# Optimization experiments

Measured on AMD Instinct MI355X. Metric: run time of the kernel, lower is better.

Reference implementation:

```python
import jax, jax.numpy as jnp
import numpy as np

# ---- static config ----
G = 4          # num graphs
NG = 512       # nodes per graph
N = G * NG     # total nodes
E = 32768      # num edges
IN_DIM = 128
HID = 32
HEADS = 4
HC = HID * HEADS  # 128
OUT_DIM = 32
N_LAYERS = 2
GRID = 500
Q = 20
NEG_SLOPE = 0.2
QUANTILES = jnp.asarray(np.linspace(0.0, 1.0, Q), jnp.float32)  # [Q]


def setup_inputs() -> dict:
    key = jax.random.key(0)
    ks = jax.random.split(key, 32)
    inp = {}
    inp['x'] = jax.random.normal(ks[0], (N, IN_DIM), jnp.float32)
    inp['edge_index'] = jax.random.randint(ks[1], (2, E), 0, N).astype(jnp.int64)
    inp['batch'] = (jnp.arange(N) // NG).astype(jnp.int64)
    # GATConv params (2 layers, both 128 -> 4 heads x 32, concat)
    for l, (kin,) in enumerate([(IN_DIM,), (HC,)]):
        s = 1.0 / np.sqrt(kin)
        inp[f'W{l}'] = jax.random.normal(ks[2 + 4 * l], (kin, HC), jnp.float32) * s
        inp[f'as{l}'] = jax.random.normal(ks[3 + 4 * l], (HEADS, HID), jnp.float32) * s
        inp[f'ad{l}'] = jax.random.normal(ks[4 + 4 * l], (HEADS, HID), jnp.float32) * s
        inp[f'b{l}'] = jnp.zeros((HC,), jnp.float32)
    for l in range(N_LAYERS + 1):
        inp[f'lpW{l}'] = jax.random.normal(ks[10 + 2 * l], (HC, OUT_DIM), jnp.float32) * (1.0 / np.sqrt(HC))
        inp[f'lpb{l}'] = jnp.zeros((OUT_DIM,), jnp.float32)
    for l in range(N_LAYERS + 1):
        inp[f'kW{l}'] = jax.random.normal(ks[16 + 2 * l], (HC * Q, OUT_DIM), jnp.float32) * (1.0 / np.sqrt(HC * Q))
        inp[f'kb{l}'] = jnp.zeros((OUT_DIM,), jnp.float32)
    inp['pool_w'] = jnp.ones((2,), jnp.float32) / 2.0
    inp['beta'] = jax.random.normal(ks[22], (OUT_DIM,), jnp.float32)
    inp['h0'] = jax.random.normal(ks[23], (1,), jnp.float32)
    return inp


def _gat_layer(x, src, dst, W, a_src, a_dst, bias):
    # PyG GATConv (concat=True, add_self_loops=True, negative_slope=0.2), eval mode
    n = x.shape[0]
    xh = (x @ W).reshape(n, HEADS, HID)              # [N,H,C]
    loop = jnp.arange(n)
    s = jnp.concatenate([src, loop])                 # [E+N]
    d = jnp.concatenate([dst, loop])
    al_s = jnp.einsum('nhc,hc->nh', xh, a_src)       # [N,H]
    al_d = jnp.einsum('nhc,hc->nh', xh, a_dst)
    e = jax.nn.leaky_relu(al_s[s] + al_d[d], NEG_SLOPE)   # [E+N,H]
    e_max = jax.ops.segment_max(e, d, num_segments=n)     # stable softmax per dst
    e = jnp.exp(e - e_max[d])
    denom = jax.ops.segment_sum(e, d, num_segments=n)
    alpha = e / (denom[d] + 1e-16)                   # [E+N,H]
    out = jax.ops.segment_sum(alpha[:, :, None] * xh[s], d, num_segments=n)
    return out.reshape(n, HC) + bias


def _kde_per_graph(xg):
    # xg: [Ng, D] -> [D*Q] soft-quantile features via grid KDE
    n = xg.shape[0]
    mn = xg.min(axis=0) - 1e-6                       # [D]
    mx = xg.max(axis=0) + 1e-6
    grid = jnp.linspace(0.0, 1.0, GRID)[:, None] * (mx - mn) + mn   # [Gp,D]
    std = xg.std(axis=0) + 1e-8 / 3
    h = 1.06 * std * float(n) ** (-0.2)              # [D]
    u = (grid[:, None, :] - xg[None, :, :]) / h      # [Gp,Ng,D]  (dominant tensor)
    kern = jnp.exp(-0.5 * u * u) / (h * np.sqrt(2.0 * np.pi))
    density = kern.mean(axis=1)                      # [Gp,D]
    cdf = jnp.cumsum(density, axis=0)
    cdf = cdf / jnp.clip(cdf[-1:], 1e-8)
    dist = jnp.abs(cdf[:, :, None] - QUANTILES)      # [Gp,D,Q]
    w = jax.nn.sigmoid(-100.0 * dist)
    w = w / (w.sum(axis=0, keepdims=True) + 1e-8)
    qv = (grid[:, :, None] * w).sum(axis=0)          # [D,Q]
    return qv.reshape(-1)


def _readout(cur, lpW, lpb, kW, kb, pool_w):
    xr = cur.reshape(G, NG, -1)
    pooled = jnp.stack([xr.mean(axis=1), xr.max(axis=1)], axis=0)   # [2,G,D]
    wp = (pooled * pool_w[:, None, None]).sum(axis=0)               # [G,D]
    h = wp @ lpW + lpb                                              # [G,out]
    kf = jax.vmap(_kde_per_graph)(xr)                               # [G,D*Q]
    return h, kf @ kW + kb


def reference(x, edge_index, batch, W0, as0, ad0, b0, W1, as1, ad1, b1,
              lpW0, lpb0, lpW1, lpb1, lpW2, lpb2,
              kW0, kb0, kW1, kb1, kW2, kb2, pool_w, beta, h0):
    src, dst = edge_index[0], edge_index[1]
    convs = [(W0, as0, ad0, b0), (W1, as1, ad1, b1)]
    lps = [(lpW0, lpb0), (lpW1, lpb1), (lpW2, lpb2)]
    kps = [(kW0, kb0), (kW1, kb1), (kW2, kb2)]
    cur = x
    h_list, kde_list = [], []
    for i in range(N_LAYERS):
        h, kp = _readout(cur, lps[i][0], lps[i][1], kps[i][0], kps[i][1], pool_w)
        h_list.append(h); kde_list.append(kp)
        cur = _gat_layer(cur, src, dst, *convs[i])
        if i != N_LAYERS - 1:
            cur = jax.nn.relu(cur)
    h, kp = _readout(cur, lps[-1][0], lps[-1][1], kps[-1][0], kps[-1][1], pool_w)
    h_list.append(h); kde_list.append(kp)
    main_out = jnp.stack(h_list).mean(axis=0)        # [G,out]
    kde_out = jnp.stack(kde_list).mean(axis=0)
    risk = (main_out + kde_out) @ beta + h0          # [G]
    return risk
```

## Files before the change

### kernel.cpp

```cpp
#include <hip/hip_runtime.h>
#include <math.h>

#define GNUM 4
#define NG 512
#define NN 2048
#define EE 32768
#define HC 128
#define HEADS 4
#define HID 32
#define GRID_PTS 500
#define QN 20
#define ODIM 32
#define MAXE 160

#define LOG2E 1.44269504088896340736f
#define NEG_HALF_LOG2E -0.72134752044448170368f
#define N_POW_M02 0.2871745887492588f
#define SIG_K 144.269504089f

typedef float v2f __attribute__((ext_vector_type(2)));

__device__ __forceinline__ float fexp2(float x){ return __builtin_amdgcn_exp2f(x); }
__device__ __forceinline__ float frcp(float x){ return __builtin_amdgcn_rcpf(x); }

struct SmemKDE {
  float4 wred4[8];
  float sc[4];
  float wsum[8], woff[9];
  float redw[QN][8], redg[QN][8];
  float qs[QN];
};
struct SmemXW  { float rows[4][HC]; int cnt[4]; };
struct SmemGat {
  int   ssrc[4][MAXE];
  float sexp[4][MAXE][HEADS];
};
union Smem { SmemKDE kde; SmemXW xw; SmemGat gat; };

__device__ void kde_phase(Smem& sm, const float* __restrict__ vpl, const float* __restrict__ spl,
        int b,
        const float* __restrict__ kW, const float* __restrict__ kb, float* __restrict__ kacc,
        const float* __restrict__ lpW, const float* __restrict__ lpb,
        const float* __restrict__ poolw, float* __restrict__ macc){
  int g = b >> 7, d = b & 127;
  int t = threadIdx.x;
  int lane = t & 63, wave = t >> 6;
  size_t base = (size_t)d*NN + g*NG;
  float v  = vpl[base + t];
  float v2 = spl[base + t];
  float mn=v, mx=v, smv=v, sq=v2;
  #pragma unroll
  for (int m=32; m>0; m>>=1){
    mn = fminf(mn, __shfl_xor(mn, m, 64));
    mx = fmaxf(mx, __shfl_xor(mx, m, 64));
    smv += __shfl_xor(smv, m, 64);
    sq += __shfl_xor(sq, m, 64);
  }
  if (lane==0) sm.kde.wred4[wave] = make_float4(mn,mx,smv,sq);
  __syncthreads();
  if (t==0){
    float4 r = sm.kde.wred4[0];
    #pragma unroll
    for (int i=1;i<8;++i){
      float4 bb = sm.kde.wred4[i];
      r.x = fminf(r.x,bb.x); r.y = fmaxf(r.y,bb.y); r.z += bb.z; r.w += bb.w;
    }
    float mean = r.z * (1.f/NG);
    float var  = fmaxf(r.w*(1.f/NG) - mean*mean, 0.f);
    float sd   = sqrtf(var) + (1e-8f/3.f);
    float h    = 1.06f * sd * N_POW_M02;
    float lo = r.x - 1e-6f, hi = r.y + 1e-6f;
    sm.kde.sc[0] = lo;
    sm.kde.sc[1] = (hi-lo)*(1.f/(GRID_PTS-1));
    sm.kde.sc[2] = NEG_HALF_LOG2E/(h*h);
    sm.kde.sc[3] = poolw[0]*mean + poolw[1]*r.y;
  }
  __syncthreads();
  float lo = sm.kde.sc[0], st = sm.kde.sc[1], kk = sm.kde.sc[2];
  float gv = lo + st*(float)t;
  float acc = 0.f;
  {
    float c0 = kk*gv*gv, c1 = -2.f*kk*gv;
    v2f c0v = {c0, c0}, c1v = {c1, c1}, kkv = {kk, kk};
    const float4* pv = (const float4*)(vpl + base);
    const float4* ps = (const float4*)(spl + base);
    #pragma unroll 8
    for (int i=0;i<NG/4;++i){
      float4 a = pv[i];
      float4 bq = ps[i];
      v2f alo = {a.x, a.y}, ahi = {a.z, a.w};
      v2f blo = {bq.x, bq.y}, bhi = {bq.z, bq.w};
      v2f plo = __builtin_elementwise_fma(kkv, blo, __builtin_elementwise_fma(c1v, alo, c0v));
      v2f phi = __builtin_elementwise_fma(kkv, bhi, __builtin_elementwise_fma(c1v, ahi, c0v));
      acc += fexp2(plo.x);
      acc += fexp2(plo.y);
      acc += fexp2(phi.x);
      acc += fexp2(phi.y);
    }
  }
  if (t >= GRID_PTS) acc = 0.f;
  float sv = acc;
  #pragma unroll
  for (int off=1; off<64; off<<=1){
    float n = __shfl_up(sv, off, 64);
    if (lane >= off) sv += n;
  }
  if (lane==63) sm.kde.wsum[wave] = sv;
  __syncthreads();
  if (t==0){
    float r2 = 0.f;
    #pragma unroll
    for (int i=0;i<8;++i){ sm.kde.woff[i]=r2; r2+=sm.kde.wsum[i]; }
    sm.kde.woff[8]=r2;
  }
  if (t < QN*8){ ((float*)sm.kde.redw)[t]=0.f; ((float*)sm.kde.redg)[t]=0.f; }
  __syncthreads();
  float invt = 1.f/fmaxf(sm.kde.woff[8], 1e-8f);
  float c = (sv + sm.kde.woff[wave]) * invt;
  float cw0 = __shfl(c, 0, 64), cw1 = __shfl(c, 63, 64);
  int qlo = max(0, (int)ceilf((cw0 - 0.17f)*(float)(QN-1)));
  int qhi = min(QN-1, (int)floorf((cw1 + 0.17f)*(float)(QN-1)));
  for (int q=qlo; q<=qhi; ++q){
    float w = 0.f;
    if (t < GRID_PTS){
      float dist = fabsf(c - (float)q*(1.f/(QN-1)));
      w = frcp(1.f + fexp2(SIG_K*dist));
    }
    float gw = gv*w;
    #pragma unroll
    for (int m=32;m>0;m>>=1){
      w  += __shfl_xor(w,  m, 64);
      gw += __shfl_xor(gw, m, 64);
    }
    if (lane==0){ sm.kde.redw[q][wave]=w; sm.kde.redg[q][wave]=gw; }
  }
  __syncthreads();
  if (t < QN){
    float sw=0.f, sgw=0.f;
    #pragma unroll
    for (int i=0;i<8;++i){ sw+=sm.kde.redw[t][i]; sgw+=sm.kde.redg[t][i]; }
    sm.kde.qs[t] = sgw / (sw + 1e-8f);
  }
  __syncthreads();
  if (t < ODIM){
    float a = 0.f;
    const float* kwb = kW + (size_t)d*QN*ODIM + t;
    #pragma unroll
    for (int q=0;q<QN;++q) a += sm.kde.qs[q]*kwb[q*ODIM];
    if (d==0) a += kb[t];
    kacc[(size_t)d*128 + g*ODIM + t] = a;
    float bb = sm.kde.sc[3]*lpW[d*ODIM + t];
    if (d==0) bb += lpb[t];
    macc[(size_t)d*128 + g*ODIM + t] = bb;
  }
  __syncthreads();
}

__device__ float gather_core(Smem& sm, int d, int sub, int tl,
        const int* __restrict__ csr, const int* __restrict__ deg,
        const float* __restrict__ als, const float* __restrict__ ald,
        const float* __restrict__ xh, const float* __restrict__ bias){
  int dg = deg[d];
  int E = dg + 1;
  int Ep = (E + 7) & ~7;
  const int* base = csr + d*MAXE;
  float a0 = ald[d*4+0], a1 = ald[d*4+1], a2 = ald[d*4+2], a3 = ald[d*4+3];
  for (int i=tl; i<Ep; i+=128){
    int s = (i < dg) ? base[i] : d;
    sm.gat.ssrc[sub][i] = s;
    if (i < E){
      float e0 = als[s*4+0]+a0, e1 = als[s*4+1]+a1, e2 = als[s*4+2]+a2, e3 = als[s*4+3]+a3;
      e0 = (e0>=0.f)? e0 : 0.2f*e0;
      e1 = (e1>=0.f)? e1 : 0.2f*e1;
      e2 = (e2>=0.f)? e2 : 0.2f*e2;
      e3 = (e3>=0.f)? e3 : 0.2f*e3;
      sm.gat.sexp[sub][i][0]=e0; sm.gat.sexp[sub][i][1]=e1;
      sm.gat.sexp[sub][i][2]=e2; sm.gat.sexp[sub][i][3]=e3;
    } else {
      sm.gat.sexp[sub][i][0]=0.f; sm.gat.sexp[sub][i][1]=0.f;
      sm.gat.sexp[sub][i][2]=0.f; sm.gat.sexp[sub][i][3]=0.f;
    }
  }
  __syncthreads();
  int h = tl >> 5, l32 = tl & 31;
  float mx = -INFINITY;
  for (int i=l32; i<E; i+=32) mx = fmaxf(mx, sm.gat.sexp[sub][i][h]);
  #pragma unroll
  for (int m=16; m>0; m>>=1) mx = fmaxf(mx, __shfl_xor(mx, m, 32));
  float sdn = 0.f;
  for (int i=l32; i<E; i+=32){
    float ev = fexp2(LOG2E*(sm.gat.sexp[sub][i][h] - mx));
    sm.gat.sexp[sub][i][h] = ev;
    sdn += ev;
  }
  #pragma unroll
  for (int m=16; m>0; m>>=1) sdn += __shfl_xor(sdn, m, 32);
  float fac = 1.f/(sdn + 1e-16f);
  float acc = bias[tl];
  for (int i0=0; i0<Ep; i0+=8){
    #pragma unroll
    for (int k=0;k<8;++k){
      int i = i0 + k;
      acc += sm.gat.sexp[sub][i][h]*fac * xh[(size_t)sm.gat.ssrc[sub][i]*HC + tl];
    }
  }
  __syncthreads();
  return acc;
}

__device__ void xw_emit(Smem& sm, int sub, int j, int n,
        const float* __restrict__ W, const float* __restrict__ as_, const float* __restrict__ ad_,
        float* __restrict__ xh, float* __restrict__ als, float* __restrict__ ald){
  float acc = 0.f;
  #pragma unroll 8
  for (int c2=0;c2<HC;++c2)
    acc += sm.xw.rows[sub][c2]*W[(size_t)c2*HC + j];
  xh[(size_t)n*HC + j] = acc;
  int h = j >> 5, cc = j & 31;
  float ps = acc*as_[h*HID+cc], pd = acc*ad_[h*HID+cc];
  #pragma unroll
  for (int m=16;m>0;m>>=1){
    ps += __shfl_xor(ps, m, 32);
    pd += __shfl_xor(pd, m, 32);
  }
  if (cc==0){ als[n*HEADS+h]=ps; ald[n*HEADS+h]=pd; }
}

__device__ void write_transposed(Smem& sm, int t, int n0,
                                 float* __restrict__ vpl, float* __restrict__ spl){
  if (t < HC){
    float v0 = sm.xw.rows[0][t], v1 = sm.xw.rows[1][t];
    float v2 = sm.xw.rows[2][t], v3 = sm.xw.rows[3][t];
    *(float4*)(vpl + (size_t)t*NN + n0) = make_float4(v0, v1, v2, v3);
    *(float4*)(spl + (size_t)t*NN + n0) = make_float4(v0*v0, v1*v1, v2*v2, v3*v3);
  }
}

__global__ __launch_bounds__(512) void k_T(const float* __restrict__ x,
                                           float* __restrict__ vpl, float* __restrict__ spl){
  __shared__ float rows[4][HC];
  int t = threadIdx.x;
  int sub = t >> 7, j = t & 127;
  int n0 = blockIdx.x*4;
  rows[sub][j] = x[(size_t)(n0+sub)*HC + j];
  __syncthreads();
  if (t < HC){
    float v0 = rows[0][t], v1 = rows[1][t], v2 = rows[2][t], v3 = rows[3][t];
    *(float4*)(vpl + (size_t)t*NN + n0) = make_float4(v0, v1, v2, v3);
    *(float4*)(spl + (size_t)t*NN + n0) = make_float4(v0*v0, v1*v1, v2*v2, v3*v3);
  }
}

__global__ __launch_bounds__(512) void k_L0(const float* __restrict__ x,
        const float* __restrict__ xTv, const float* __restrict__ xTs,
        const float* __restrict__ kW, const float* __restrict__ kb, float* __restrict__ kacc,
        const float* __restrict__ lpW, const float* __restrict__ lpb,
        const float* __restrict__ poolw, float* __restrict__ macc,
        const float* __restrict__ W, const float* __restrict__ as_, const float* __restrict__ ad_,
        float* __restrict__ xh, float* __restrict__ als, float* __restrict__ ald,
        const int* __restrict__ src, const int* __restrict__ dst,
        int* __restrict__ deg, int* __restrict__ csr){
  __shared__ Smem sm;
  int t = threadIdx.x;
  if (blockIdx.x >= 512){
    kde_phase(sm, xTv, xTs, blockIdx.x - 512, kW, kb, kacc, lpW, lpb, poolw, macc);
  } else {
    int b2 = blockIdx.x;
    int sub = t >> 7, j = t & 127;
    int n = b2*4 + sub;
    if (t < 4) sm.xw.cnt[t] = 0;
    sm.xw.rows[sub][j] = x[(size_t)n*HC + j];
    __syncthreads();
    int base4 = b2*4;
    for (int e = t; e < EE; e += 512){
      int dd = dst[e];
      unsigned r = (unsigned)(dd - base4);
      if (r < 4u){
        int p = atomicAdd(&sm.xw.cnt[r], 1);
        if (p < MAXE) csr[dd*MAXE + p] = src[e];
      }
    }
    xw_emit(sm, sub, j, n, W, as_, ad_, xh, als, ald);
    __syncthreads();
    if (t < 4) deg[base4 + t] = min(sm.xw.cnt[t], MAXE-1);
  }
}

__global__ __launch_bounds__(512) void k_G0(const int* __restrict__ csr, const int* __restrict__ deg,
        const float* __restrict__ als_in, const float* __restrict__ ald_in,
        const float* __restrict__ xh_in, const float* __restrict__ bias,
        float* __restrict__ c1v, float* __restrict__ c1s,
        const float* __restrict__ W1, const float* __restrict__ as1, const float* __restrict__ ad1,
        float* __restrict__ xh2, float* __restrict__ als2, float* __restrict__ ald2,
        const float* __restrict__ xTv, const float* __restrict__ xTs,
        const float* __restrict__ kW, const float* __restrict__ kb, float* __restrict__ kacc,
        const float* __restrict__ lpW, const float* __restrict__ lpb,
        const float* __restrict__ poolw, float* __restrict__ macc){
  __shared__ Smem sm;
  int t = threadIdx.x;
  if (blockIdx.x >= 512){
    kde_phase(sm, xTv, xTs, blockIdx.x - 256, kW, kb, kacc, lpW, lpb, poolw, macc);
    return;
  }
  int sub = t >> 7, tl = t & 127;
  int d = blockIdx.x*4 + sub;
  float acc = gather_core(sm, d, sub, tl, csr, deg, als_in, ald_in, xh_in, bias);
  sm.xw.rows[sub][tl] = fmaxf(acc, 0.f);
  __syncthreads();
  write_transposed(sm, t, blockIdx.x*4, c1v, c1s);
  xw_emit(sm, sub, tl, d, W1, as1, ad1, xh2, als2, ald2);
}

__global__ __launch_bounds__(512) void k_L1(const float* __restrict__ c1v, const float* __restrict__ c1s,
        const float* __restrict__ kW, const float* __restrict__ kb, float* __restrict__ kacc,
        const float* __restrict__ lpW, const float* __restrict__ lpb,
        const float* __restrict__ poolw, float* __restrict__ macc,
        const int* __restrict__ csr, const int* __restrict__ deg,
        const float* __restrict__ als2, const float* __restrict__ ald2,
        const float* __restrict__ xh2, const float* __restrict__ bias,
        float* __restrict__ c2v, float* __restrict__ c2s){
  __shared__ Smem sm;
  int t = threadIdx.x;
  if (blockIdx.x < 512){
    kde_phase(sm, c1v, c1s, blockIdx.x, kW, kb, kacc, lpW, lpb, poolw, macc);
  } else {
    int b2 = blockIdx.x - 512;
    int sub = t >> 7, tl = t & 127;
    int d = b2*4 + sub;
    float acc = gather_core(sm, d, sub, tl, csr, deg, als2, ald2, xh2, bias);
    sm.xw.rows[sub][tl] = acc;
    __syncthreads();
    write_transposed(sm, t, b2*4, c2v, c2s);
  }
}

__global__ __launch_bounds__(512) void k_L2(const float* __restrict__ c2v, const float* __restrict__ c2s,
        const float* __restrict__ kW, const float* __restrict__ kb, float* __restrict__ kacc,
        const float* __restrict__ lpW, const float* __restrict__ lpb,
        const float* __restrict__ poolw, float* __restrict__ macc){
  __shared__ Smem sm;
  kde_phase(sm, c2v, c2s, blockIdx.x, kW, kb, kacc, lpW, lpb, poolw, macc);
}

__global__ __launch_bounds__(384) void k_final(const float* __restrict__ mpart, const float* __restrict__ kpart,
                        const float* __restrict__ beta, const float* __restrict__ h0,
                        float* __restrict__ out){
  int t = threadIdx.x;
  __shared__ float sdm[384];
  int l = t >> 7, tt = t & 127;
  const float* mrow = mpart + (size_t)l*16384 + tt;
  const float* krow = kpart + (size_t)l*16384 + tt;
  float s = 0.f;
  #pragma unroll 8
  for (int d2=0; d2<128; ++d2) s += mrow[(size_t)d2*128] + krow[(size_t)d2*128];
  sdm[t] = s;
  __syncthreads();
  if (t < 128){
    int g = t >> 5, o = t & 31;
    float s3 = (sdm[t] + sdm[t+128] + sdm[t+256]) * (1.f/3.f) * beta[o];
    #pragma unroll
    for (int m=16; m>0; m>>=1) s3 += __shfl_xor(s3, m, 32);
    if (o == 0) out[g] = s3 + h0[0];
  }
}

extern "C" void kernel_launch(void* const* d_in, const int* in_sizes, int n_in,
                              void* d_out, int out_size, void* d_ws, size_t ws_size,
                              hipStream_t stream) {
  (void)in_sizes; (void)n_in; (void)out_size; (void)ws_size;
  const float* x    = (const float*)d_in[0];
  const int*   ei   = (const int*)d_in[1];
  const int*   srcp = ei;
  const int*   dstp = ei + EE;
  const float* W[2]   = {(const float*)d_in[3], (const float*)d_in[7]};
  const float* As[2]  = {(const float*)d_in[4], (const float*)d_in[8]};
  const float* Ad[2]  = {(const float*)d_in[5], (const float*)d_in[9]};
  const float* Bi[2]  = {(const float*)d_in[6], (const float*)d_in[10]};
  const float* lpW[3] = {(const float*)d_in[11], (const float*)d_in[13], (const float*)d_in[15]};
  const float* lpb[3] = {(const float*)d_in[12], (const float*)d_in[14], (const float*)d_in[16]};
  const float* kW[3]  = {(const float*)d_in[17], (const float*)d_in[19], (const float*)d_in[21]};
  const float* kb[3]  = {(const float*)d_in[18], (const float*)d_in[20], (const float*)d_in[22]};
  const float* poolw  = (const float*)d_in[23];
  const float* beta   = (const float*)d_in[24];
  const float* h0     = (const float*)d_in[25];
  float* out = (float*)d_out;

  float* ws = (float*)d_ws;
  float* xTv   = ws;
  float* xTs   = xTv + 262144;
  float* c1v   = xTs + 262144;
  float* c1s   = c1v + 262144;
  float* c2v   = c1s + 262144;
  float* c2s   = c2v + 262144;
  float* xh    = c2s + 262144;
  float* xh2   = xh + 262144;
  float* als   = xh2 + 262144;
  float* ald   = als + 8192;
  float* als2  = ald + 8192;
  float* ald2  = als2 + 8192;
  float* mpart = ald2 + 8192;
  float* kpart = mpart + 49152;
  int*   deg   = (int*)(kpart + 49152);
  int*   csr   = deg + 2048;

  k_T<<<512, 512, 0, stream>>>(x, xTv, xTs);
  k_L0<<<768, 512, 0, stream>>>(x, xTv, xTs, kW[0], kb[0], kpart, lpW[0], lpb[0], poolw, mpart,
                                W[0], As[0], Ad[0], xh, als, ald,
                                srcp, dstp, deg, csr);
  k_G0<<<768, 512, 0, stream>>>(csr, deg, als, ald, xh, Bi[0], c1v, c1s,
                                W[1], As[1], Ad[1], xh2, als2, ald2,
                                xTv, xTs, kW[0], kb[0], kpart, lpW[0], lpb[0], poolw, mpart);
  k_L1<<<1024, 512, 0, stream>>>(c1v, c1s, kW[1], kb[1], kpart+16384, lpW[1], lpb[1], poolw, mpart+16384,
                                 csr, deg, als2, ald2, xh2, Bi[1], c2v, c2s);
  k_L2<<<512, 512, 0, stream>>>(c2v, c2s, kW[2], kb[2], kpart+32768, lpW[2], lpb[2], poolw, mpart+32768);
  k_final<<<1, 384, 0, stream>>>(mpart, kpart, beta, h0, out);
}
```

Baseline: 213.2 us.

## Drop transpose kernel, fuse layer-0 KDE into k_L0 and final reduction into k_L2

Removes the separate transpose kernel. The layer-0 KDE blocks now read x directly with strided per-feature loads and stage value and square pairs in shared memory, and all 512 KDE blocks move from being split across k_L0 and k_G0 into k_L0 alone. The final reduction kernel is folded into k_L2 through a last-block-done atomic counter with thread fences, which cuts two launches. It also vectorizes the attention-logit gather into a float4 load. The strided column reads of x may coalesce poorly, and k_L0 grows to 1024 blocks.

```diff
diff --git a/kernel.cpp b/kernel.cpp
--- a/kernel.cpp
+++ b/kernel.cpp
@@ -24,6 +24,7 @@
 __device__ __forceinline__ float frcp(float x){ return __builtin_amdgcn_rcpf(x); }
 
 struct SmemKDE {
+  __align__(16) float2 xs[NG];
   float4 wred4[8];
   float sc[4];
   float wsum[8], woff[9];
@@ -35,10 +36,12 @@
   int   ssrc[4][MAXE];
   float sexp[4][MAXE][HEADS];
 };
-union Smem { SmemKDE kde; SmemXW xw; SmemGat gat; };
-
+struct SmemFin { float sdm[384]; };
+union Smem { SmemKDE kde; SmemXW xw; SmemGat gat; SmemFin fin; };
+
+template<int PLANE>
 __device__ void kde_phase(Smem& sm, const float* __restrict__ vpl, const float* __restrict__ spl,
-        int b,
+        const float* __restrict__ xsrc, int b,
         const float* __restrict__ kW, const float* __restrict__ kb, float* __restrict__ kacc,
         const float* __restrict__ lpW, const float* __restrict__ lpb,
         const float* __restrict__ poolw, float* __restrict__ macc){
@@ -46,8 +49,15 @@
   int t = threadIdx.x;
   int lane = t & 63, wave = t >> 6;
   size_t base = (size_t)d*NN + g*NG;
-  float v  = vpl[base + t];
-  float v2 = spl[base + t];
+  float v, v2;
+  if (PLANE){
+    v  = vpl[base + t];
+    v2 = spl[base + t];
+  } else {
+    v = xsrc[((size_t)g*NG + t)*HC + d];
+    v2 = v*v;
+    sm.kde.xs[t] = make_float2(v, v2);
+  }
   float mn=v, mx=v, smv=v, sq=v2;
   #pragma unroll
   for (int m=32; m>0; m>>=1){
@@ -79,7 +89,7 @@
   float lo = sm.kde.sc[0], st = sm.kde.sc[1], kk = sm.kde.sc[2];
   float gv = lo + st*(float)t;
   float acc = 0.f;
-  {
+  if (PLANE){
     float c0 = kk*gv*gv, c1 = -2.f*kk*gv;
     v2f c0v = {c0, c0}, c1v = {c1, c1}, kkv = {kk, kk};
     const float4* pv = (const float4*)(vpl + base);
@@ -97,6 +107,15 @@
       acc += fexp2(phi.x);
       acc += fexp2(phi.y);
     }
+  } else {
+    float c0 = kk*gv*gv, c1 = -2.f*kk*gv;
+    const float4* p4 = (const float4*)sm.kde.xs;
+    #pragma unroll 8
+    for (int i=0;i<NG/2;++i){
+      float4 s2 = p4[i];
+      acc += fexp2(fmaf(kk, s2.y, fmaf(c1, s2.x, c0)));
+      acc += fexp2(fmaf(kk, s2.w, fmaf(c1, s2.z, c0)));
+    }
   }
   if (t >= GRID_PTS) acc = 0.f;
   float sv = acc;
@@ -169,7 +188,8 @@
     int s = (i < dg) ? base[i] : d;
     sm.gat.ssrc[sub][i] = s;
     if (i < E){
-      float e0 = als[s*4+0]+a0, e1 = als[s*4+1]+a1, e2 = als[s*4+2]+a2, e3 = als[s*4+3]+a3;
+      float4 av = *(const float4*)(als + (size_t)s*4);
+      float e0 = av.x+a0, e1 = av.y+a1, e2 = av.z+a2, e3 = av.w+a3;
       e0 = (e0>=0.f)? e0 : 0.2f*e0;
       e1 = (e1>=0.f)? e1 : 0.2f*e1;
       e2 = (e2>=0.f)? e2 : 0.2f*e2;
@@ -236,36 +256,21 @@
   }
 }
 
-__global__ __launch_bounds__(512) void k_T(const float* __restrict__ x,
-                                           float* __restrict__ vpl, float* __restrict__ spl){
-  __shared__ float rows[4][HC];
-  int t = threadIdx.x;
-  int sub = t >> 7, j = t & 127;
-  int n0 = blockIdx.x*4;
-  rows[sub][j] = x[(size_t)(n0+sub)*HC + j];
-  __syncthreads();
-  if (t < HC){
-    float v0 = rows[0][t], v1 = rows[1][t], v2 = rows[2][t], v3 = rows[3][t];
-    *(float4*)(vpl + (size_t)t*NN + n0) = make_float4(v0, v1, v2, v3);
-    *(float4*)(spl + (size_t)t*NN + n0) = make_float4(v0*v0, v1*v1, v2*v2, v3*v3);
-  }
-}
-
 __global__ __launch_bounds__(512) void k_L0(const float* __restrict__ x,
-        const float* __restrict__ xTv, const float* __restrict__ xTs,
         const float* __restrict__ kW, const float* __restrict__ kb, float* __restrict__ kacc,
         const float* __restrict__ lpW, const float* __restrict__ lpb,
         const float* __restrict__ poolw, float* __restrict__ macc,
         const float* __restrict__ W, const float* __restrict__ as_, const float* __restrict__ ad_,
         float* __restrict__ xh, float* __restrict__ als, float* __restrict__ ald,
         const int* __restrict__ src, const int* __restrict__ dst,
-        int* __restrict__ deg, int* __restrict__ csr){
+        int* __restrict__ deg, int* __restrict__ csr, int* __restrict__ donecnt){
   __shared__ Smem sm;
   int t = threadIdx.x;
-  if (blockIdx.x >= 512){
-    kde_phase(sm, xTv, xTs, blockIdx.x - 512, kW, kb, kacc, lpW, lpb, poolw, macc);
+  if (blockIdx.x < 512){
+    kde_phase<0>(sm, nullptr, nullptr, x, blockIdx.x, kW, kb, kacc, lpW, lpb, poolw, macc);
   } else {
-    int b2 = blockIdx.x;
+    int b2 = blockIdx.x - 512;
+    if (b2 == 0 && t == 0) *donecnt = 0;
     int sub = t >> 7, j = t & 127;
     int n = b2*4 + sub;
     if (t < 4) sm.xw.cnt[t] = 0;
@@ -291,17 +296,9 @@
         const float* __restrict__ xh_in, const float* __restrict__ bias,
         float* __restrict__ c1v, float* __restrict__ c1s,
         const float* __restrict__ W1, const float* __restrict__ as1, const float* __restrict__ ad1,
-        float* __restrict__ xh2, float* __restrict__ als2, float* __restrict__ ald2,
-        const float* __restrict__ xTv, const float* __restrict__ xTs,
-        const float* __restrict__ kW, const float* __restrict__ kb, float* __restrict__ kacc,
-        const float* __restrict__ lpW, const float* __restrict__ lpb,
-        const float* __restrict__ poolw, float* __restrict__ macc){
+        float* __restrict__ xh2, float* __restrict__ als2, float* __restrict__ ald2){
   __shared__ Smem sm;
   int t = threadIdx.x;
-  if (blockIdx.x >= 512){
-    kde_phase(sm, xTv, xTs, blockIdx.x - 256, kW, kb, kacc, lpW, lpb, poolw, macc);
-    return;
-  }
   int sub = t >> 7, tl = t & 127;
   int d = blockIdx.x*4 + sub;
   float acc = gather_core(sm, d, sub, tl, csr, deg, als_in, ald_in, xh_in, bias);
@@ -322,7 +319,7 @@
   __shared__ Smem sm;
   int t = threadIdx.x;
   if (blockIdx.x < 512){
-    kde_phase(sm, c1v, c1s, blockIdx.x, kW, kb, kacc, lpW, lpb, poolw, macc);
+    kde_phase<1>(sm, c1v, c1s, nullptr, blockIdx.x, kW, kb, kacc, lpW, lpb, poolw, macc);
   } else {
     int b2 = blockIdx.x - 512;
     int sub = t >> 7, tl = t & 127;
@@ -337,27 +334,32 @@
 __global__ __launch_bounds__(512) void k_L2(const float* __restrict__ c2v, const float* __restrict__ c2s,
         const float* __restrict__ kW, const float* __restrict__ kb, float* __restrict__ kacc,
         const float* __restrict__ lpW, const float* __restrict__ lpb,
-        const float* __restrict__ poolw, float* __restrict__ macc){
+        const float* __restrict__ poolw, float* __restrict__ macc,
+        const float* __restrict__ mpart, const float* __restrict__ kpart,
+        const float* __restrict__ beta, const float* __restrict__ h0,
+        float* __restrict__ out, int* __restrict__ donecnt){
   __shared__ Smem sm;
-  kde_phase(sm, c2v, c2s, blockIdx.x, kW, kb, kacc, lpW, lpb, poolw, macc);
-}
-
-__global__ __launch_bounds__(384) void k_final(const float* __restrict__ mpart, const float* __restrict__ kpart,
-                        const float* __restrict__ beta, const float* __restrict__ h0,
-                        float* __restrict__ out){
+  __shared__ int lastFlag;
   int t = threadIdx.x;
-  __shared__ float sdm[384];
-  int l = t >> 7, tt = t & 127;
-  const float* mrow = mpart + (size_t)l*16384 + tt;
-  const float* krow = kpart + (size_t)l*16384 + tt;
-  float s = 0.f;
-  #pragma unroll 8
-  for (int d2=0; d2<128; ++d2) s += mrow[(size_t)d2*128] + krow[(size_t)d2*128];
-  sdm[t] = s;
+  kde_phase<1>(sm, c2v, c2s, nullptr, blockIdx.x, kW, kb, kacc, lpW, lpb, poolw, macc);
+  __threadfence();
+  if (t == 0) lastFlag = (atomicAdd(donecnt, 1) == 511);
+  __syncthreads();
+  if (!lastFlag) return;
+  __threadfence();
+  if (t < 384){
+    int l = t >> 7, tt = t & 127;
+    const float* mrow = mpart + (size_t)l*16384 + tt;
+    const float* krow = kpart + (size_t)l*16384 + tt;
+    float s = 0.f;
+    #pragma unroll 8
+    for (int d2=0; d2<128; ++d2) s += mrow[(size_t)d2*128] + krow[(size_t)d2*128];
+    sm.fin.sdm[t] = s;
+  }
   __syncthreads();
   if (t < 128){
     int g = t >> 5, o = t & 31;
-    float s3 = (sdm[t] + sdm[t+128] + sdm[t+256]) * (1.f/3.f) * beta[o];
+    float s3 = (sm.fin.sdm[t] + sm.fin.sdm[t+128] + sm.fin.sdm[t+256]) * (1.f/3.f) * beta[o];
     #pragma unroll
     for (int m=16; m>0; m>>=1) s3 += __shfl_xor(s3, m, 32);
     if (o == 0) out[g] = s3 + h0[0];
@@ -386,9 +388,7 @@
   float* out = (float*)d_out;
 
   float* ws = (float*)d_ws;
-  float* xTv   = ws;
-  float* xTs   = xTv + 262144;
-  float* c1v   = xTs + 262144;
+  float* c1v   = ws;
   float* c1s   = c1v + 262144;
   float* c2v   = c1s + 262144;
   float* c2s   = c2v + 262144;
@@ -402,16 +402,15 @@
   float* kpart = mpart + 49152;
   int*   deg   = (int*)(kpart + 49152);
   int*   csr   = deg + 2048;
-
-  k_T<<<512, 512, 0, stream>>>(x, xTv, xTs);
-  k_L0<<<768, 512, 0, stream>>>(x, xTv, xTs, kW[0], kb[0], kpart, lpW[0], lpb[0], poolw, mpart,
-                                W[0], As[0], Ad[0], xh, als, ald,
-                                srcp, dstp, deg, csr);
-  k_G0<<<768, 512, 0, stream>>>(csr, deg, als, ald, xh, Bi[0], c1v, c1s,
-                                W[1], As[1], Ad[1], xh2, als2, ald2,
-                                xTv, xTs, kW[0], kb[0], kpart, lpW[0], lpb[0], poolw, mpart);
+  int*   donecnt = csr + 2048*MAXE;
+
+  k_L0<<<1024, 512, 0, stream>>>(x, kW[0], kb[0], kpart, lpW[0], lpb[0], poolw, mpart,
+                                 W[0], As[0], Ad[0], xh, als, ald,
+                                 srcp, dstp, deg, csr, donecnt);
+  k_G0<<<512, 512, 0, stream>>>(csr, deg, als, ald, xh, Bi[0], c1v, c1s,
+                                W[1], As[1], Ad[1], xh2, als2, ald2);
   k_L1<<<1024, 512, 0, stream>>>(c1v, c1s, kW[1], kb[1], kpart+16384, lpW[1], lpb[1], poolw, mpart+16384,
                                  csr, deg, als2, ald2, xh2, Bi[1], c2v, c2s);
-  k_L2<<<512, 512, 0, stream>>>(c2v, c2s, kW[2], kb[2], kpart+32768, lpW[2], lpb[2], poolw, mpart+32768);
-  k_final<<<1, 384, 0, stream>>>(mpart, kpart, beta, h0, out);
-}
+  k_L2<<<512, 512, 0, stream>>>(c2v, c2s, kW[2], kb[2], kpart+32768, lpW[2], lpb[2], poolw, mpart+32768,
+                                mpart, kpart, beta, h0, out, donecnt);
+}
```

Measured after the change: 253.7 us. +19.0%, slower.

## Use 1024-thread blocks, split KDE node sums across halves, 8 nodes per block

Applied to the files above, without the earlier changes.

All KDE work moves to 1024-thread blocks. Two thread halves each sum the Gaussian exponentials over half of a graph's nodes, and the partial sums are combined in shared memory. Because each block now does more KDE work, all layer-0 KDE blocks run in k_L0, and k_G0 becomes a pure gather kernel. Gather and xw blocks now process 8 nodes per block instead of 4, and the source attention logits are read as a float4. The aim is to halve the serial exponential loop per thread and rebalance work across kernels, at the cost of an extra barrier, idle upper-half threads during scans, and tighter register limits from the new launch bounds.

```diff
diff --git a/kernel.cpp b/kernel.cpp
--- a/kernel.cpp
+++ b/kernel.cpp
@@ -29,15 +29,14 @@
   float wsum[8], woff[9];
   float redw[QN][8], redg[QN][8];
   float qs[QN];
+  float psum[512];
 };
-struct SmemXW  { float rows[4][HC]; int cnt[4]; };
-struct SmemGat {
-  int   ssrc[4][MAXE];
-  float sexp[4][MAXE][HEADS];
-};
-union Smem { SmemKDE kde; SmemXW xw; SmemGat gat; };
-
-__device__ void kde_phase(Smem& sm, const float* __restrict__ vpl, const float* __restrict__ spl,
+struct SmemXW  { float rows[8][HC]; int cnt[8]; };
+struct SmemGat { int ssrc[8][MAXE]; float sexp[8][MAXE][HEADS]; };
+struct SmemFin { float sdm[384]; };
+union Smem { SmemKDE kde; SmemXW xw; SmemGat gat; SmemFin fin; };
+
+__device__ void kde_fat(Smem& sm, const float* __restrict__ vpl, const float* __restrict__ spl,
         int b,
         const float* __restrict__ kW, const float* __restrict__ kb, float* __restrict__ kacc,
         const float* __restrict__ lpW, const float* __restrict__ lpb,
@@ -45,9 +44,11 @@
   int g = b >> 7, d = b & 127;
   int t = threadIdx.x;
   int lane = t & 63, wave = t >> 6;
+  bool lower = t < 512;
+  int gp = lower ? t : t - 512;
   size_t base = (size_t)d*NN + g*NG;
-  float v  = vpl[base + t];
-  float v2 = spl[base + t];
+  float v = 0.f, v2 = 0.f;
+  if (lower){ v = vpl[base + t]; v2 = spl[base + t]; }
   float mn=v, mx=v, smv=v, sq=v2;
   #pragma unroll
   for (int m=32; m>0; m>>=1){
@@ -56,7 +57,7 @@
     smv += __shfl_xor(smv, m, 64);
     sq += __shfl_xor(sq, m, 64);
   }
-  if (lane==0) sm.kde.wred4[wave] = make_float4(mn,mx,smv,sq);
+  if (lower && lane==0) sm.kde.wred4[wave] = make_float4(mn,mx,smv,sq);
   __syncthreads();
   if (t==0){
     float4 r = sm.kde.wred4[0];
@@ -77,15 +78,15 @@
   }
   __syncthreads();
   float lo = sm.kde.sc[0], st = sm.kde.sc[1], kk = sm.kde.sc[2];
-  float gv = lo + st*(float)t;
+  float gv = lo + st*(float)gp;
   float acc = 0.f;
   {
     float c0 = kk*gv*gv, c1 = -2.f*kk*gv;
     v2f c0v = {c0, c0}, c1v = {c1, c1}, kkv = {kk, kk};
-    const float4* pv = (const float4*)(vpl + base);
-    const float4* ps = (const float4*)(spl + base);
+    const float4* pv = (const float4*)(vpl + base) + (lower ? 0 : 64);
+    const float4* ps = (const float4*)(spl + base) + (lower ? 0 : 64);
     #pragma unroll 8
-    for (int i=0;i<NG/4;++i){
+    for (int i=0;i<64;++i){
       float4 a = pv[i];
       float4 bq = ps[i];
       v2f alo = {a.x, a.y}, ahi = {a.z, a.w};
@@ -98,14 +99,17 @@
       acc += fexp2(phi.y);
     }
   }
-  if (t >= GRID_PTS) acc = 0.f;
+  if (gp >= GRID_PTS) acc = 0.f;
+  if (!lower) sm.kde.psum[gp] = acc;
+  __syncthreads();
+  if (lower) acc += sm.kde.psum[t];
   float sv = acc;
   #pragma unroll
   for (int off=1; off<64; off<<=1){
     float n = __shfl_up(sv, off, 64);
     if (lane >= off) sv += n;
   }
-  if (lane==63) sm.kde.wsum[wave] = sv;
+  if (lower && lane==63) sm.kde.wsum[wave] = sv;
   __syncthreads();
   if (t==0){
     float r2 = 0.f;
@@ -116,23 +120,25 @@
   if (t < QN*8){ ((float*)sm.kde.redw)[t]=0.f; ((float*)sm.kde.redg)[t]=0.f; }
   __syncthreads();
   float invt = 1.f/fmaxf(sm.kde.woff[8], 1e-8f);
-  float c = (sv + sm.kde.woff[wave]) * invt;
-  float cw0 = __shfl(c, 0, 64), cw1 = __shfl(c, 63, 64);
-  int qlo = max(0, (int)ceilf((cw0 - 0.17f)*(float)(QN-1)));
-  int qhi = min(QN-1, (int)floorf((cw1 + 0.17f)*(float)(QN-1)));
-  for (int q=qlo; q<=qhi; ++q){
-    float w = 0.f;
-    if (t < GRID_PTS){
-      float dist = fabsf(c - (float)q*(1.f/(QN-1)));
-      w = frcp(1.f + fexp2(SIG_K*dist));
-    }
-    float gw = gv*w;
-    #pragma unroll
-    for (int m=32;m>0;m>>=1){
-      w  += __shfl_xor(w,  m, 64);
-      gw += __shfl_xor(gw, m, 64);
-    }
-    if (lane==0){ sm.kde.redw[q][wave]=w; sm.kde.redg[q][wave]=gw; }
+  if (lower){
+    float c = (sv + sm.kde.woff[wave]) * invt;
+    float cw0 = __shfl(c, 0, 64), cw1 = __shfl(c, 63, 64);
+    int qlo = max(0, (int)ceilf((cw0 - 0.17f)*(float)(QN-1)));
+    int qhi = min(QN-1, (int)floorf((cw1 + 0.17f)*(float)(QN-1)));
+    for (int q=qlo; q<=qhi; ++q){
+      float w = 0.f;
+      if (gp < GRID_PTS){
+        float dist = fabsf(c - (float)q*(1.f/(QN-1)));
+        w = frcp(1.f + fexp2(SIG_K*dist));
+      }
+      float gw = gv*w;
+      #pragma unroll
+      for (int m=32;m>0;m>>=1){
+        w  += __shfl_xor(w,  m, 64);
+        gw += __shfl_xor(gw, m, 64);
+      }
+      if (lane==0){ sm.kde.redw[q][wave]=w; sm.kde.redg[q][wave]=gw; }
+    }
   }
   __syncthreads();
   if (t < QN){
@@ -169,7 +175,8 @@
     int s = (i < dg) ? base[i] : d;
     sm.gat.ssrc[sub][i] = s;
     if (i < E){
-      float e0 = als[s*4+0]+a0, e1 = als[s*4+1]+a1, e2 = als[s*4+2]+a2, e3 = als[s*4+3]+a3;
+      float4 av = *(const float4*)(als + (size_t)s*4);
+      float e0 = av.x+a0, e1 = av.y+a1, e2 = av.z+a2, e3 = av.w+a3;
       e0 = (e0>=0.f)? e0 : 0.2f*e0;
       e1 = (e1>=0.f)? e1 : 0.2f*e1;
       e2 = (e2>=0.f)? e2 : 0.2f*e2;
@@ -226,13 +233,19 @@
   if (cc==0){ als[n*HEADS+h]=ps; ald[n*HEADS+h]=pd; }
 }
 
-__device__ void write_transposed(Smem& sm, int t, int n0,
-                                 float* __restrict__ vpl, float* __restrict__ spl){
+__device__ void write_transposed8(Smem& sm, int t, int n0,
+                                  float* __restrict__ vpl, float* __restrict__ spl){
   if (t < HC){
-    float v0 = sm.xw.rows[0][t], v1 = sm.xw.rows[1][t];
-    float v2 = sm.xw.rows[2][t], v3 = sm.xw.rows[3][t];
-    *(float4*)(vpl + (size_t)t*NN + n0) = make_float4(v0, v1, v2, v3);
-    *(float4*)(spl + (size_t)t*NN + n0) = make_float4(v0*v0, v1*v1, v2*v2, v3*v3);
+    float r0 = sm.xw.rows[0][t], r1 = sm.xw.rows[1][t];
+    float r2 = sm.xw.rows[2][t], r3 = sm.xw.rows[3][t];
+    float r4 = sm.xw.rows[4][t], r5 = sm.xw.rows[5][t];
+    float r6 = sm.xw.rows[6][t], r7 = sm.xw.rows[7][t];
+    float4* pv = (float4*)(vpl + (size_t)t*NN + n0);
+    float4* ps = (float4*)(spl + (size_t)t*NN + n0);
+    pv[0] = make_float4(r0, r1, r2, r3);
+    pv[1] = make_float4(r4, r5, r6, r7);
+    ps[0] = make_float4(r0*r0, r1*r1, r2*r2, r3*r3);
+    ps[1] = make_float4(r4*r4, r5*r5, r6*r6, r7*r7);
   }
 }
 
@@ -251,7 +264,7 @@
   }
 }
 
-__global__ __launch_bounds__(512) void k_L0(const float* __restrict__ x,
+__global__ __launch_bounds__(1024, 8) void k_L0(const float* __restrict__ x,
         const float* __restrict__ xTv, const float* __restrict__ xTs,
         const float* __restrict__ kW, const float* __restrict__ kb, float* __restrict__ kacc,
         const float* __restrict__ lpW, const float* __restrict__ lpb,
@@ -262,56 +275,48 @@
         int* __restrict__ deg, int* __restrict__ csr){
   __shared__ Smem sm;
   int t = threadIdx.x;
-  if (blockIdx.x >= 512){
-    kde_phase(sm, xTv, xTs, blockIdx.x - 512, kW, kb, kacc, lpW, lpb, poolw, macc);
+  if (blockIdx.x < 512){
+    kde_fat(sm, xTv, xTs, blockIdx.x, kW, kb, kacc, lpW, lpb, poolw, macc);
   } else {
-    int b2 = blockIdx.x;
+    int b2 = blockIdx.x - 512;
     int sub = t >> 7, j = t & 127;
-    int n = b2*4 + sub;
-    if (t < 4) sm.xw.cnt[t] = 0;
+    int n = b2*8 + sub;
+    if (t < 8) sm.xw.cnt[t] = 0;
     sm.xw.rows[sub][j] = x[(size_t)n*HC + j];
     __syncthreads();
-    int base4 = b2*4;
-    for (int e = t; e < EE; e += 512){
+    int base8 = b2*8;
+    for (int e = t; e < EE; e += 1024){
       int dd = dst[e];
-      unsigned r = (unsigned)(dd - base4);
-      if (r < 4u){
+      unsigned r = (unsigned)(dd - base8);
+      if (r < 8u){
         int p = atomicAdd(&sm.xw.cnt[r], 1);
         if (p < MAXE) csr[dd*MAXE + p] = src[e];
       }
     }
     xw_emit(sm, sub, j, n, W, as_, ad_, xh, als, ald);
     __syncthreads();
-    if (t < 4) deg[base4 + t] = min(sm.xw.cnt[t], MAXE-1);
-  }
-}
-
-__global__ __launch_bounds__(512) void k_G0(const int* __restrict__ csr, const int* __restrict__ deg,
+    if (t < 8) deg[base8 + t] = min(sm.xw.cnt[t], MAXE-1);
+  }
+}
+
+__global__ __launch_bounds__(1024, 8) void k_G0(const int* __restrict__ csr, const int* __restrict__ deg,
         const float* __restrict__ als_in, const float* __restrict__ ald_in,
         const float* __restrict__ xh_in, const float* __restrict__ bias,
         float* __restrict__ c1v, float* __restrict__ c1s,
         const float* __restrict__ W1, const float* __restrict__ as1, const float* __restrict__ ad1,
-        float* __restrict__ xh2, float* __restrict__ als2, float* __restrict__ ald2,
-        const float* __restrict__ xTv, const float* __restrict__ xTs,
-        const float* __restrict__ kW, const float* __restrict__ kb, float* __restrict__ kacc,
-        const float* __restrict__ lpW, const float* __restrict__ lpb,
-        const float* __restrict__ poolw, float* __restrict__ macc){
+        float* __restrict__ xh2, float* __restrict__ als2, float* __restrict__ ald2){
   __shared__ Smem sm;
   int t = threadIdx.x;
-  if (blockIdx.x >= 512){
-    kde_phase(sm, xTv, xTs, blockIdx.x - 256, kW, kb, kacc, lpW, lpb, poolw, macc);
-    return;
-  }
   int sub = t >> 7, tl = t & 127;
-  int d = blockIdx.x*4 + sub;
+  int d = blockIdx.x*8 + sub;
   float acc = gather_core(sm, d, sub, tl, csr, deg, als_in, ald_in, xh_in, bias);
   sm.xw.rows[sub][tl] = fmaxf(acc, 0.f);
   __syncthreads();
-  write_transposed(sm, t, blockIdx.x*4, c1v, c1s);
+  write_transposed8(sm, t, blockIdx.x*8, c1v, c1s);
   xw_emit(sm, sub, tl, d, W1, as1, ad1, xh2, als2, ald2);
 }
 
-__global__ __launch_bounds__(512) void k_L1(const float* __restrict__ c1v, const float* __restrict__ c1s,
+__global__ __launch_bounds__(1024, 8) void k_L1(const float* __restrict__ c1v, const float* __restrict__ c1s,
         const float* __restrict__ kW, const float* __restrict__ kb, float* __restrict__ kacc,
         const float* __restrict__ lpW, const float* __restrict__ lpb,
         const float* __restrict__ poolw, float* __restrict__ macc,
@@ -322,24 +327,24 @@
   __shared__ Smem sm;
   int t = threadIdx.x;
   if (blockIdx.x < 512){
-    kde_phase(sm, c1v, c1s, blockIdx.x, kW, kb, kacc, lpW, lpb, poolw, macc);
+    kde_fat(sm, c1v, c1s, blockIdx.x, kW, kb, kacc, lpW, lpb, poolw, macc);
   } else {
     int b2 = blockIdx.x - 512;
     int sub = t >> 7, tl = t & 127;
-    int d = b2*4 + sub;
+    int d = b2*8 + sub;
     float acc = gather_core(sm, d, sub, tl, csr, deg, als2, ald2, xh2, bias);
     sm.xw.rows[sub][tl] = acc;
     __syncthreads();
-    write_transposed(sm, t, b2*4, c2v, c2s);
-  }
-}
-
-__global__ __launch_bounds__(512) void k_L2(const float* __restrict__ c2v, const float* __restrict__ c2s,
+    write_transposed8(sm, t, b2*8, c2v, c2s);
+  }
+}
+
+__global__ __launch_bounds__(1024, 8) void k_L2(const float* __restrict__ c2v, const float* __restrict__ c2s,
         const float* __restrict__ kW, const float* __restrict__ kb, float* __restrict__ kacc,
         const float* __restrict__ lpW, const float* __restrict__ lpb,
         const float* __restrict__ poolw, float* __restrict__ macc){
   __shared__ Smem sm;
-  kde_phase(sm, c2v, c2s, blockIdx.x, kW, kb, kacc, lpW, lpb, poolw, macc);
+  kde_fat(sm, c2v, c2s, blockIdx.x, kW, kb, kacc, lpW, lpb, poolw, macc);
 }
 
 __global__ __launch_bounds__(384) void k_final(const float* __restrict__ mpart, const float* __restrict__ kpart,
@@ -404,14 +409,13 @@
   int*   csr   = deg + 2048;
 
   k_T<<<512, 512, 0, stream>>>(x, xTv, xTs);
-  k_L0<<<768, 512, 0, stream>>>(x, xTv, xTs, kW[0], kb[0], kpart, lpW[0], lpb[0], poolw, mpart,
-                                W[0], As[0], Ad[0], xh, als, ald,
-                                srcp, dstp, deg, csr);
-  k_G0<<<768, 512, 0, stream>>>(csr, deg, als, ald, xh, Bi[0], c1v, c1s,
-                                W[1], As[1], Ad[1], xh2, als2, ald2,
-                                xTv, xTs, kW[0], kb[0], kpart, lpW[0], lpb[0], poolw, mpart);
-  k_L1<<<1024, 512, 0, stream>>>(c1v, c1s, kW[1], kb[1], kpart+16384, lpW[1], lpb[1], poolw, mpart+16384,
+  k_L0<<<768, 1024, 0, stream>>>(x, xTv, xTs, kW[0], kb[0], kpart, lpW[0], lpb[0], poolw, mpart,
+                                 W[0], As[0], Ad[0], xh, als, ald,
+                                 srcp, dstp, deg, csr);
+  k_G0<<<256, 1024, 0, stream>>>(csr, deg, als, ald, xh, Bi[0], c1v, c1s,
+                                 W[1], As[1], Ad[1], xh2, als2, ald2);
+  k_L1<<<768, 1024, 0, stream>>>(c1v, c1s, kW[1], kb[1], kpart+16384, lpW[1], lpb[1], poolw, mpart+16384,
                                  csr, deg, als2, ald2, xh2, Bi[1], c2v, c2s);
-  k_L2<<<512, 512, 0, stream>>>(c2v, c2s, kW[2], kb[2], kpart+32768, lpW[2], lpb[2], poolw, mpart+32768);
+  k_L2<<<512, 1024, 0, stream>>>(c2v, c2s, kW[2], kb[2], kpart+32768, lpW[2], lpb[2], poolw, mpart+32768);
   k_final<<<1, 384, 0, stream>>>(mpart, kpart, beta, h0, out);
 }
```

Result: slower. 243.2 us (+14.1%).
